# Performance work log

Measured on AMD Instinct MI355X. Metric: run time of the kernel, lower is better.

## Reference

```python
import math
import jax, jax.numpy as jnp
import numpy as np

B, H, S, D = 8, 16, 1024, 64

def setup_inputs() -> dict:
    key = jax.random.key(0)
    kq, kk, kv, km = jax.random.split(key, 4)
    query = jax.random.normal(kq, (B, H, S, D), dtype=jnp.float32)
    k_ = jax.random.normal(kk, (B, H, S, D), dtype=jnp.float32)
    value = jax.random.normal(kv, (B, H, S, D), dtype=jnp.float32)
    mask = jax.random.randint(km, (B, 1, S, S), 0, 2).astype(jnp.bool_)
    return {"query": query, "key": k_, "value": value, "mask": mask}

def reference(query, key, value, mask) -> jnp.ndarray:
    dk = query.shape[-1]
    # scores: [B,H,S,S]
    scores = jnp.einsum("bhqd,bhkd->bhqk", query, key) / math.sqrt(dk)
    scores = jnp.where(mask, scores, jnp.float32(-1e9))
    attention = jax.nn.softmax(scores, axis=-1)
    # log(sigmoid(v)) computed stably, then exp of the weighted sum
    logsig_v = jax.nn.log_sigmoid(value)  # [B,H,S,D]
    return jnp.exp(jnp.einsum("bhqk,bhkd->bhqd", attention, logsig_v))
```

## Files before the change

### kernel.cpp

```cpp
#include <hip/hip_runtime.h>

typedef _Float16 half8  __attribute__((ext_vector_type(8)));
typedef _Float16 half2v __attribute__((ext_vector_type(2)));
typedef float    f32x16 __attribute__((ext_vector_type(16)));
typedef float    f32x4v __attribute__((ext_vector_type(4)));

namespace {
constexpr int kB = 8, kH = 16, kS = 1024, kD = 64;
constexpr int QT  = 128;
constexpr int KT  = 64;
constexpr int NKT = kS / KT;
constexpr int KST = 72;
}

__global__ __launch_bounds__(256, 2)
void sdpa_logsig_kernel(const float* __restrict__ Qg_, const float* __restrict__ Kg_,
                        const float* __restrict__ Vg_, const void* __restrict__ Mg_,
                        float* __restrict__ Og_) {
  __shared__ _Float16 Klds[KT][KST];
  __shared__ _Float16 Vlds[kD][KST];
  __shared__ _Float16 Ptl[4][32][KST];

  const int t    = threadIdx.x;
  const int qblk = blockIdx.x;
  const int bh   = blockIdx.y;
  const int b    = bh >> 4;

  const float* Qg = Qg_ + ((size_t)bh * kS + (size_t)qblk * QT) * kD;
  const float* Kg = Kg_ + (size_t)bh * kS * kD;
  const float* Vg = Vg_ + (size_t)bh * kS * kD;
  float* Og = Og_ + ((size_t)bh * kS + (size_t)qblk * QT) * kD;

  const int l    = t & 63;
  const int w    = t >> 6;
  const int h    = l >> 5;
  const int q31  = l & 31;
  const int qloc = w * 32 + q31;
  const int qg   = qblk * QT + qloc;

  const int skey = t >> 2;
  const int sj   = t & 3;
  const int sd4  = sj << 4;

  unsigned pacc = 0;
  {
    const unsigned* mprobe = (const unsigned*)Mg_;
    #pragma unroll
    for (int i = 0; i < 16; ++i) pacc |= mprobe[i] & 0xFFFFFF00u;
  }
  const bool mask_i32 = (pacc == 0);
  const size_t moff0 = (size_t)b * kS * kS + (size_t)qg * kS + 4 * h;

  half8 qf[4];
  {
    const float* qp = Qg + (size_t)qloc * kD + 8 * h;
    #pragma unroll
    for (int c = 0; c < 4; ++c) {
      f32x4v x = *(const f32x4v*)(qp + 16 * c);
      f32x4v y = *(const f32x4v*)(qp + 16 * c + 4);
      half8 f;
      #pragma unroll
      for (int j = 0; j < 4; ++j) {
        f[j]     = (_Float16)(x[j] * 0.125f);
        f[j + 4] = (_Float16)(y[j] * 0.125f);
      }
      qf[c] = f;
    }
  }

  f32x16 oacc[2];
  #pragma unroll
  for (int d = 0; d < 2; ++d) {
    #pragma unroll
    for (int i = 0; i < 16; ++i) oacc[d][i] = 0.f;
  }
  float mrun = -1e9f, lrun = 0.f;

  for (int kt = 0; kt < NKT; ++kt) {
    __syncthreads();

    {
      const float* kp = Kg + (size_t)(kt * KT + skey) * kD + sd4;
      f32x4v a0 = *(const f32x4v*)(kp);
      f32x4v a1 = *(const f32x4v*)(kp + 4);
      f32x4v a2 = *(const f32x4v*)(kp + 8);
      f32x4v a3 = *(const f32x4v*)(kp + 12);
      half8 h0, h1;
      #pragma unroll
      for (int j = 0; j < 4; ++j) {
        h0[j] = (_Float16)a0[j]; h0[j + 4] = (_Float16)a1[j];
        h1[j] = (_Float16)a2[j]; h1[j + 4] = (_Float16)a3[j];
      }
      *(half8*)&Klds[skey][sd4]     = h0;
      *(half8*)&Klds[skey][sd4 + 8] = h1;
    }

    {
      const float* vp = Vg + (size_t)(kt * KT + skey) * kD + sd4;
      _Float16 lv[16];
      #pragma unroll
      for (int i = 0; i < 4; ++i) {
        const int c = (i + sj) & 3;
        f32x4v xv = *(const f32x4v*)(vp + 4 * c);
        #pragma unroll
        for (int jj = 0; jj < 4; ++jj) {
          float x  = xv[jj];
          float ls = fminf(x, 0.f) - __logf(1.f + __expf(-fabsf(x)));
          lv[4 * i + jj] = (_Float16)ls;
        }
      }
      #pragma unroll
      for (int i = 0; i < 4; ++i) {
        const int c = (i + sj) & 3;
        #pragma unroll
        for (int jj = 0; jj < 4; ++jj)
          Vlds[sd4 + 4 * c + jj][skey] = lv[4 * i + jj];
      }
    }

    unsigned mq[8];
    if (mask_i32) {
      const int* mp = (const int*)Mg_ + moff0 + kt * KT;
      #pragma unroll
      for (int i = 0; i < 8; ++i) {
        const int4 mv = *(const int4*)(mp + 32 * (i >> 2) + 8 * (i & 3));
        mq[i] = (unsigned)(mv.x & 1) | ((unsigned)(mv.y & 1) << 8) |
                ((unsigned)(mv.z & 1) << 16) | ((unsigned)(mv.w & 1) << 24);
      }
    } else {
      const unsigned char* mp = (const unsigned char*)Mg_ + moff0 + kt * KT;
      #pragma unroll
      for (int i = 0; i < 8; ++i)
        mq[i] = *(const unsigned*)(mp + 32 * (i >> 2) + 8 * (i & 3));
    }
    __syncthreads();

    f32x16 sacc[2];
    #pragma unroll
    for (int ks = 0; ks < 2; ++ks) {
      #pragma unroll
      for (int i = 0; i < 16; ++i) sacc[ks][i] = 0.f;
    }
    #pragma unroll
    for (int ks = 0; ks < 2; ++ks) {
      #pragma unroll
      for (int c = 0; c < 4; ++c) {
        half8 kf = *(const half8*)&Klds[32 * ks + q31][16 * c + 8 * h];
        sacc[ks] = __builtin_amdgcn_mfma_f32_32x32x16_f16(kf, qf[c], sacc[ks], 0, 0, 0);
      }
    }

    float smax = -1e9f;
    #pragma unroll
    for (int ks = 0; ks < 2; ++ks) {
      #pragma unroll
      for (int m4 = 0; m4 < 4; ++m4) {
        const unsigned mw = mq[4 * ks + m4];
        #pragma unroll
        for (int r = 0; r < 4; ++r) {
          float s = sacc[ks][4 * m4 + r];
          s = ((mw >> (8 * r)) & 0xffu) ? s : -1e9f;
          sacc[ks][4 * m4 + r] = s;
          smax = fmaxf(smax, s);
        }
      }
    }
    smax = fmaxf(smax, __shfl_xor(smax, 32));
    const float mnew = fmaxf(mrun, smax);
    const float corr = __expf(mrun - mnew);
    mrun = mnew;

    float psum = 0.f;
    #pragma unroll
    for (int ks = 0; ks < 2; ++ks) {
      #pragma unroll
      for (int m4 = 0; m4 < 4; ++m4) {
        _Float16 p0 = (_Float16)__expf(sacc[ks][4 * m4 + 0] - mnew);
        _Float16 p1 = (_Float16)__expf(sacc[ks][4 * m4 + 1] - mnew);
        _Float16 p2 = (_Float16)__expf(sacc[ks][4 * m4 + 2] - mnew);
        _Float16 p3 = (_Float16)__expf(sacc[ks][4 * m4 + 3] - mnew);
        psum += (float)p0 + (float)p1 + (float)p2 + (float)p3;
        half2v p01; p01[0] = p0; p01[1] = p1;
        half2v p23; p23[0] = p2; p23[1] = p3;
        const int key0 = 32 * ks + 8 * m4 + 4 * h;
        *(half2v*)&Ptl[w][q31][key0]     = p01;
        *(half2v*)&Ptl[w][q31][key0 + 2] = p23;
      }
    }
    psum += __shfl_xor(psum, 32);
    lrun = lrun * corr + psum;
    #pragma unroll
    for (int d = 0; d < 2; ++d) {
      #pragma unroll
      for (int i = 0; i < 16; ++i) oacc[d][i] *= corr;
    }

    half8 pf[4];
    #pragma unroll
    for (int c2 = 0; c2 < 4; ++c2)
      pf[c2] = *(const half8*)&Ptl[w][q31][16 * c2 + 8 * h];
    #pragma unroll
    for (int ds = 0; ds < 2; ++ds) {
      #pragma unroll
      for (int c2 = 0; c2 < 4; ++c2) {
        half8 vf = *(const half8*)&Vlds[32 * ds + q31][16 * c2 + 8 * h];
        oacc[ds] = __builtin_amdgcn_mfma_f32_32x32x16_f16(vf, pf[c2], oacc[ds], 0, 0, 0);
      }
    }
  }

  const float invl = 1.f / lrun;
  float* op = Og + (size_t)qloc * kD;
  #pragma unroll
  for (int ds = 0; ds < 2; ++ds) {
    #pragma unroll
    for (int m4 = 0; m4 < 4; ++m4) {
      f32x4v v;
      #pragma unroll
      for (int r = 0; r < 4; ++r)
        v[r] = __expf(oacc[ds][4 * m4 + r] * invl);
      *(f32x4v*)&op[32 * ds + 8 * m4 + 4 * h] = v;
    }
  }
}

extern "C" void kernel_launch(void* const* d_in, const int* in_sizes, int n_in,
                              void* d_out, int out_size, void* d_ws, size_t ws_size,
                              hipStream_t stream) {
  const float* Q = (const float*)d_in[0];
  const float* K = (const float*)d_in[1];
  const float* V = (const float*)d_in[2];
  const void*  M = (const void*)d_in[3];
  float* O = (float*)d_out;
  dim3 grid(kS / QT, kB * kH);
  sdpa_logsig_kernel<<<grid, dim3(256), 0, stream>>>(Q, K, V, M, O);
}
```

Baseline: 262.8 us.

## Precompute fp16 K, transposed log-sigmoid V and packed mask bits in a prepass

Adds a preprocessing kernel that writes K as fp16, log-sigmoid(V) as transposed fp16, and the int mask as 32-bit bitmasks into the workspace. The attention kernel then reads these compact arrays instead of re-reading fp32 K/V and the full int mask for every query block and every head. The main kernel also adds register double-buffering of the next tile, an XCD-aware block index mapping, and raises launch bounds to 4 blocks per CU. The cost is an extra launch plus a full pass over K, V and the mask. The prepass assumes an int32 mask layout and drops the byte-mask detection the old kernel did.

```diff
diff --git a/kernel.cpp b/kernel.cpp
--- a/kernel.cpp
+++ b/kernel.cpp
@@ -1,6 +1,7 @@
 #include <hip/hip_runtime.h>
 
 typedef _Float16 half8  __attribute__((ext_vector_type(8)));
+typedef _Float16 half4v __attribute__((ext_vector_type(4)));
 typedef _Float16 half2v __attribute__((ext_vector_type(2)));
 typedef float    f32x16 __attribute__((ext_vector_type(16)));
 typedef float    f32x4v __attribute__((ext_vector_type(4)));
@@ -11,6 +12,240 @@
 constexpr int KT  = 64;
 constexpr int NKT = kS / KT;
 constexpr int KST = 72;
+constexpr size_t KH_OFF = 0;
+constexpr size_t VT_OFF = (size_t)kB * kH * kS * kD * 2;
+constexpr size_t MB_OFF = VT_OFF * 2;
+constexpr size_t WS_NEED = MB_OFF + (size_t)kB * kS * (kS / 32) * 4;
+}
+
+__device__ __forceinline__ float logsig(float x) {
+  return fminf(x, 0.f) - __logf(1.f + __expf(-fabsf(x)));
+}
+
+__global__ __launch_bounds__(256, 4)
+void pre_kernel(const float* __restrict__ K, const float* __restrict__ V,
+                const int* __restrict__ M, _Float16* __restrict__ Kh,
+                _Float16* __restrict__ Vt, unsigned* __restrict__ Mb) {
+  const int blk = blockIdx.x, t = threadIdx.x;
+  if (blk < 8192) {
+    const size_t idx = ((size_t)blk * 256 + t) * 4;
+    f32x4v x = *(const f32x4v*)(K + idx);
+    half4v o;
+    #pragma unroll
+    for (int j = 0; j < 4; ++j) o[j] = (_Float16)x[j];
+    *(half4v*)(Kh + idx) = o;
+  } else if (blk < 10240) {
+    __shared__ _Float16 T[64][72];
+    const int bb = blk - 8192;
+    const int bh = bb >> 4, ktt = bb & 15;
+    const int key = t >> 2, dc = (t & 3) << 4;
+    const float* vp = V + (((size_t)bh * kS + ktt * KT + key)) * kD + dc;
+    #pragma unroll
+    for (int i = 0; i < 4; ++i) {
+      f32x4v x = *(const f32x4v*)(vp + 4 * i);
+      #pragma unroll
+      for (int j = 0; j < 4; ++j) T[dc + 4 * i + j][key] = (_Float16)logsig(x[j]);
+    }
+    __syncthreads();
+    const int d = t >> 2, kc = (t & 3) << 4;
+    half8 r0 = *(const half8*)&T[d][kc];
+    half8 r1 = *(const half8*)&T[d][kc + 8];
+    _Float16* op = Vt + ((size_t)bh * kD + d) * kS + ktt * KT + kc;
+    *(half8*)op = r0;
+    *(half8*)(op + 8) = r1;
+  } else {
+    const int wi = (blk - 10240) * 256 + t;
+    const int row = wi >> 5;
+    const int wrd = wi & 31;
+    const int* mp = M + (size_t)row * kS + wrd * 32;
+    unsigned bits = 0;
+    #pragma unroll
+    for (int i = 0; i < 8; ++i) {
+      const int4 v = *(const int4*)(mp + 4 * i);
+      bits |= (unsigned)(v.x & 1) << (4 * i) | (unsigned)(v.y & 1) << (4 * i + 1) |
+              (unsigned)(v.z & 1) << (4 * i + 2) | (unsigned)(v.w & 1) << (4 * i + 3);
+    }
+    Mb[wi] = bits;
+  }
+}
+
+__global__ __launch_bounds__(256, 4)
+void sdpa_main(const float* __restrict__ Qg_, const _Float16* __restrict__ Kh,
+               const _Float16* __restrict__ Vt, const unsigned* __restrict__ Mb,
+               float* __restrict__ Og_) {
+  __shared__ _Float16 Klds[KT][KST];
+  __shared__ _Float16 Vlds[kD][KST];
+  __shared__ _Float16 Ptl[4][32][KST];
+
+  const int t = threadIdx.x;
+  const int n   = blockIdx.x;
+  const int xcd = n & 7, c = n >> 3;
+  const int bh  = (xcd << 4) | (c >> 3);
+  const int qblk = c & 7;
+  const int b   = bh >> 4;
+
+  const float* Qg = Qg_ + ((size_t)bh * kS + (size_t)qblk * QT) * kD;
+  float* Og = Og_ + ((size_t)bh * kS + (size_t)qblk * QT) * kD;
+
+  const int l    = t & 63;
+  const int w    = t >> 6;
+  const int h    = l >> 5;
+  const int q31  = l & 31;
+  const int qloc = w * 32 + q31;
+  const int qg   = qblk * QT + qloc;
+
+  const int skey = t >> 2;
+  const int sd4  = (t & 3) << 4;
+  const int vrow = t >> 2;
+  const int vkc  = (t & 3) << 4;
+
+  const _Float16* kbase = Kh + ((size_t)bh * kS + skey) * kD + sd4;
+  const _Float16* vbase = Vt + ((size_t)bh * kD + vrow) * kS + vkc;
+  const unsigned* mbase = Mb + ((size_t)(b * kS + qg)) * 32;
+
+  half8 qf[4];
+  {
+    const float* qp = Qg + (size_t)qloc * kD + 8 * h;
+    #pragma unroll
+    for (int cc = 0; cc < 4; ++cc) {
+      f32x4v x = *(const f32x4v*)(qp + 16 * cc);
+      f32x4v y = *(const f32x4v*)(qp + 16 * cc + 4);
+      half8 f;
+      #pragma unroll
+      for (int j = 0; j < 4; ++j) {
+        f[j]     = (_Float16)(x[j] * 0.125f);
+        f[j + 4] = (_Float16)(y[j] * 0.125f);
+      }
+      qf[cc] = f;
+    }
+  }
+
+  f32x16 oacc[2];
+  #pragma unroll
+  for (int d = 0; d < 2; ++d) {
+    #pragma unroll
+    for (int i = 0; i < 16; ++i) oacc[d][i] = 0.f;
+  }
+  float mrun = -1e9f, lrun = 0.f;
+
+  uint4 kreg0 = *(const uint4*)(kbase);
+  uint4 kreg1 = *(const uint4*)(kbase + 8);
+  uint4 vreg0 = *(const uint4*)(vbase);
+  uint4 vreg1 = *(const uint4*)(vbase + 8);
+  uint2 mreg  = *(const uint2*)(mbase);
+
+  for (int kt = 0; kt < NKT; ++kt) {
+    __syncthreads();
+
+    *(uint4*)&Klds[skey][sd4]     = kreg0;
+    *(uint4*)&Klds[skey][sd4 + 8] = kreg1;
+    *(uint4*)&Vlds[vrow][vkc]     = vreg0;
+    *(uint4*)&Vlds[vrow][vkc + 8] = vreg1;
+
+    unsigned nib[8];
+    #pragma unroll
+    for (int i = 0; i < 8; ++i) {
+      const unsigned wv = (i >> 2) ? mreg.y : mreg.x;
+      nib[i] = (wv >> (8 * (i & 3) + 4 * h)) & 0xFu;
+    }
+
+    if (kt + 1 < NKT) {
+      const size_t ko = (size_t)(kt + 1) * KT * kD;
+      kreg0 = *(const uint4*)(kbase + ko);
+      kreg1 = *(const uint4*)(kbase + ko + 8);
+      vreg0 = *(const uint4*)(vbase + (kt + 1) * KT);
+      vreg1 = *(const uint4*)(vbase + (kt + 1) * KT + 8);
+      mreg  = *(const uint2*)(mbase + (kt + 1) * 2);
+    }
+    __syncthreads();
+
+    f32x16 sacc[2];
+    #pragma unroll
+    for (int ks = 0; ks < 2; ++ks) {
+      #pragma unroll
+      for (int i = 0; i < 16; ++i) sacc[ks][i] = 0.f;
+    }
+    #pragma unroll
+    for (int ks = 0; ks < 2; ++ks) {
+      #pragma unroll
+      for (int cc = 0; cc < 4; ++cc) {
+        half8 kf = *(const half8*)&Klds[32 * ks + q31][16 * cc + 8 * h];
+        sacc[ks] = __builtin_amdgcn_mfma_f32_32x32x16_f16(kf, qf[cc], sacc[ks], 0, 0, 0);
+      }
+    }
+
+    float smax = -1e9f;
+    #pragma unroll
+    for (int ks = 0; ks < 2; ++ks) {
+      #pragma unroll
+      for (int m4 = 0; m4 < 4; ++m4) {
+        const unsigned nb = nib[4 * ks + m4];
+        #pragma unroll
+        for (int r = 0; r < 4; ++r) {
+          float s = sacc[ks][4 * m4 + r];
+          s = (nb & (1u << r)) ? s : -1e9f;
+          sacc[ks][4 * m4 + r] = s;
+          smax = fmaxf(smax, s);
+        }
+      }
+    }
+    smax = fmaxf(smax, __shfl_xor(smax, 32));
+    const float mnew = fmaxf(mrun, smax);
+    const float corr = __expf(mrun - mnew);
+    mrun = mnew;
+
+    float psum = 0.f;
+    #pragma unroll
+    for (int ks = 0; ks < 2; ++ks) {
+      #pragma unroll
+      for (int m4 = 0; m4 < 4; ++m4) {
+        float e0 = __expf(sacc[ks][4 * m4 + 0] - mnew);
+        float e1 = __expf(sacc[ks][4 * m4 + 1] - mnew);
+        float e2 = __expf(sacc[ks][4 * m4 + 2] - mnew);
+        float e3 = __expf(sacc[ks][4 * m4 + 3] - mnew);
+        psum += (e0 + e1) + (e2 + e3);
+        half2v p01; p01[0] = (_Float16)e0; p01[1] = (_Float16)e1;
+        half2v p23; p23[0] = (_Float16)e2; p23[1] = (_Float16)e3;
+        const int key0 = 32 * ks + 8 * m4 + 4 * h;
+        *(half2v*)&Ptl[w][q31][key0]     = p01;
+        *(half2v*)&Ptl[w][q31][key0 + 2] = p23;
+      }
+    }
+    psum += __shfl_xor(psum, 32);
+    lrun = lrun * corr + psum;
+    #pragma unroll
+    for (int d = 0; d < 2; ++d) {
+      #pragma unroll
+      for (int i = 0; i < 16; ++i) oacc[d][i] *= corr;
+    }
+
+    half8 pf[4];
+    #pragma unroll
+    for (int c2 = 0; c2 < 4; ++c2)
+      pf[c2] = *(const half8*)&Ptl[w][q31][16 * c2 + 8 * h];
+    #pragma unroll
+    for (int ds = 0; ds < 2; ++ds) {
+      #pragma unroll
+      for (int c2 = 0; c2 < 4; ++c2) {
+        half8 vf = *(const half8*)&Vlds[32 * ds + q31][16 * c2 + 8 * h];
+        oacc[ds] = __builtin_amdgcn_mfma_f32_32x32x16_f16(vf, pf[c2], oacc[ds], 0, 0, 0);
+      }
+    }
+  }
+
+  const float invl = 1.f / lrun;
+  float* op = Og + (size_t)qloc * kD;
+  #pragma unroll
+  for (int ds = 0; ds < 2; ++ds) {
+    #pragma unroll
+    for (int m4 = 0; m4 < 4; ++m4) {
+      f32x4v v;
+      #pragma unroll
+      for (int r = 0; r < 4; ++r)
+        v[r] = __expf(oacc[ds][4 * m4 + r] * invl);
+      *(f32x4v*)&op[32 * ds + 8 * m4 + 4 * h] = v;
+    }
+  }
 }
 
 __global__ __launch_bounds__(256, 2)
@@ -21,26 +256,20 @@
   __shared__ _Float16 Vlds[kD][KST];
   __shared__ _Float16 Ptl[4][32][KST];
 
-  const int t    = threadIdx.x;
+  const int t = threadIdx.x;
   const int qblk = blockIdx.x;
-  const int bh   = blockIdx.y;
-  const int b    = bh >> 4;
+  const int bh = blockIdx.y;
+  const int b = bh >> 4;
 
   const float* Qg = Qg_ + ((size_t)bh * kS + (size_t)qblk * QT) * kD;
   const float* Kg = Kg_ + (size_t)bh * kS * kD;
   const float* Vg = Vg_ + (size_t)bh * kS * kD;
   float* Og = Og_ + ((size_t)bh * kS + (size_t)qblk * QT) * kD;
 
-  const int l    = t & 63;
-  const int w    = t >> 6;
-  const int h    = l >> 5;
-  const int q31  = l & 31;
+  const int l = t & 63, w = t >> 6, h = l >> 5, q31 = l & 31;
   const int qloc = w * 32 + q31;
-  const int qg   = qblk * QT + qloc;
-
-  const int skey = t >> 2;
-  const int sj   = t & 3;
-  const int sd4  = sj << 4;
+  const int qg = qblk * QT + qloc;
+  const int skey = t >> 2, sj = t & 3, sd4 = sj << 4;
 
   unsigned pacc = 0;
   {
@@ -55,19 +284,15 @@
   {
     const float* qp = Qg + (size_t)qloc * kD + 8 * h;
     #pragma unroll
-    for (int c = 0; c < 4; ++c) {
-      f32x4v x = *(const f32x4v*)(qp + 16 * c);
-      f32x4v y = *(const f32x4v*)(qp + 16 * c + 4);
+    for (int cc = 0; cc < 4; ++cc) {
+      f32x4v x = *(const f32x4v*)(qp + 16 * cc);
+      f32x4v y = *(const f32x4v*)(qp + 16 * cc + 4);
       half8 f;
       #pragma unroll
-      for (int j = 0; j < 4; ++j) {
-        f[j]     = (_Float16)(x[j] * 0.125f);
-        f[j + 4] = (_Float16)(y[j] * 0.125f);
-      }
-      qf[c] = f;
-    }
-  }
-
+      for (int j = 0; j < 4; ++j) { f[j] = (_Float16)(x[j] * 0.125f); f[j + 4] = (_Float16)(y[j] * 0.125f); }
+      qf[cc] = f;
+    }
+  }
   f32x16 oacc[2];
   #pragma unroll
   for (int d = 0; d < 2; ++d) {
@@ -78,46 +303,32 @@
 
   for (int kt = 0; kt < NKT; ++kt) {
     __syncthreads();
-
     {
       const float* kp = Kg + (size_t)(kt * KT + skey) * kD + sd4;
-      f32x4v a0 = *(const f32x4v*)(kp);
-      f32x4v a1 = *(const f32x4v*)(kp + 4);
-      f32x4v a2 = *(const f32x4v*)(kp + 8);
-      f32x4v a3 = *(const f32x4v*)(kp + 12);
+      f32x4v a0 = *(const f32x4v*)(kp);     f32x4v a1 = *(const f32x4v*)(kp + 4);
+      f32x4v a2 = *(const f32x4v*)(kp + 8); f32x4v a3 = *(const f32x4v*)(kp + 12);
       half8 h0, h1;
       #pragma unroll
-      for (int j = 0; j < 4; ++j) {
-        h0[j] = (_Float16)a0[j]; h0[j + 4] = (_Float16)a1[j];
-        h1[j] = (_Float16)a2[j]; h1[j + 4] = (_Float16)a3[j];
-      }
-      *(half8*)&Klds[skey][sd4]     = h0;
-      *(half8*)&Klds[skey][sd4 + 8] = h1;
-    }
-
+      for (int j = 0; j < 4; ++j) { h0[j] = (_Float16)a0[j]; h0[j+4] = (_Float16)a1[j]; h1[j] = (_Float16)a2[j]; h1[j+4] = (_Float16)a3[j]; }
+      *(half8*)&Klds[skey][sd4] = h0; *(half8*)&Klds[skey][sd4 + 8] = h1;
+    }
     {
       const float* vp = Vg + (size_t)(kt * KT + skey) * kD + sd4;
       _Float16 lv[16];
       #pragma unroll
       for (int i = 0; i < 4; ++i) {
-        const int c = (i + sj) & 3;
-        f32x4v xv = *(const f32x4v*)(vp + 4 * c);
+        const int cc = (i + sj) & 3;
+        f32x4v xv = *(const f32x4v*)(vp + 4 * cc);
         #pragma unroll
-        for (int jj = 0; jj < 4; ++jj) {
-          float x  = xv[jj];
-          float ls = fminf(x, 0.f) - __logf(1.f + __expf(-fabsf(x)));
-          lv[4 * i + jj] = (_Float16)ls;
-        }
+        for (int jj = 0; jj < 4; ++jj) lv[4 * i + jj] = (_Float16)logsig(xv[jj]);
       }
       #pragma unroll
       for (int i = 0; i < 4; ++i) {
-        const int c = (i + sj) & 3;
+        const int cc = (i + sj) & 3;
         #pragma unroll
-        for (int jj = 0; jj < 4; ++jj)
-          Vlds[sd4 + 4 * c + jj][skey] = lv[4 * i + jj];
-      }
-    }
-
+        for (int jj = 0; jj < 4; ++jj) Vlds[sd4 + 4 * cc + jj][skey] = lv[4 * i + jj];
+      }
+    }
     unsigned mq[8];
     if (mask_i32) {
       const int* mp = (const int*)Mg_ + moff0 + kt * KT;
@@ -130,8 +341,7 @@
     } else {
       const unsigned char* mp = (const unsigned char*)Mg_ + moff0 + kt * KT;
       #pragma unroll
-      for (int i = 0; i < 8; ++i)
-        mq[i] = *(const unsigned*)(mp + 32 * (i >> 2) + 8 * (i & 3));
+      for (int i = 0; i < 8; ++i) mq[i] = *(const unsigned*)(mp + 32 * (i >> 2) + 8 * (i & 3));
     }
     __syncthreads();
 
@@ -144,12 +354,11 @@
     #pragma unroll
     for (int ks = 0; ks < 2; ++ks) {
       #pragma unroll
-      for (int c = 0; c < 4; ++c) {
-        half8 kf = *(const half8*)&Klds[32 * ks + q31][16 * c + 8 * h];
-        sacc[ks] = __builtin_amdgcn_mfma_f32_32x32x16_f16(kf, qf[c], sacc[ks], 0, 0, 0);
-      }
-    }
-
+      for (int cc = 0; cc < 4; ++cc) {
+        half8 kf = *(const half8*)&Klds[32 * ks + q31][16 * cc + 8 * h];
+        sacc[ks] = __builtin_amdgcn_mfma_f32_32x32x16_f16(kf, qf[cc], sacc[ks], 0, 0, 0);
+      }
+    }
     float smax = -1e9f;
     #pragma unroll
     for (int ks = 0; ks < 2; ++ks) {
@@ -169,21 +378,20 @@
     const float mnew = fmaxf(mrun, smax);
     const float corr = __expf(mrun - mnew);
     mrun = mnew;
-
     float psum = 0.f;
     #pragma unroll
     for (int ks = 0; ks < 2; ++ks) {
       #pragma unroll
       for (int m4 = 0; m4 < 4; ++m4) {
-        _Float16 p0 = (_Float16)__expf(sacc[ks][4 * m4 + 0] - mnew);
-        _Float16 p1 = (_Float16)__expf(sacc[ks][4 * m4 + 1] - mnew);
-        _Float16 p2 = (_Float16)__expf(sacc[ks][4 * m4 + 2] - mnew);
-        _Float16 p3 = (_Float16)__expf(sacc[ks][4 * m4 + 3] - mnew);
+        _Float16 p0 = (_Float16)__expf(sacc[ks][4*m4+0] - mnew);
+        _Float16 p1 = (_Float16)__expf(sacc[ks][4*m4+1] - mnew);
+        _Float16 p2 = (_Float16)__expf(sacc[ks][4*m4+2] - mnew);
+        _Float16 p3 = (_Float16)__expf(sacc[ks][4*m4+3] - mnew);
         psum += (float)p0 + (float)p1 + (float)p2 + (float)p3;
         half2v p01; p01[0] = p0; p01[1] = p1;
         half2v p23; p23[0] = p2; p23[1] = p3;
         const int key0 = 32 * ks + 8 * m4 + 4 * h;
-        *(half2v*)&Ptl[w][q31][key0]     = p01;
+        *(half2v*)&Ptl[w][q31][key0] = p01;
         *(half2v*)&Ptl[w][q31][key0 + 2] = p23;
       }
     }
@@ -197,8 +405,7 @@
 
     half8 pf[4];
     #pragma unroll
-    for (int c2 = 0; c2 < 4; ++c2)
-      pf[c2] = *(const half8*)&Ptl[w][q31][16 * c2 + 8 * h];
+    for (int c2 = 0; c2 < 4; ++c2) pf[c2] = *(const half8*)&Ptl[w][q31][16 * c2 + 8 * h];
     #pragma unroll
     for (int ds = 0; ds < 2; ++ds) {
       #pragma unroll
@@ -208,7 +415,6 @@
       }
     }
   }
-
   const float invl = 1.f / lrun;
   float* op = Og + (size_t)qloc * kD;
   #pragma unroll
@@ -217,8 +423,7 @@
     for (int m4 = 0; m4 < 4; ++m4) {
       f32x4v v;
       #pragma unroll
-      for (int r = 0; r < 4; ++r)
-        v[r] = __expf(oacc[ds][4 * m4 + r] * invl);
+      for (int r = 0; r < 4; ++r) v[r] = __expf(oacc[ds][4 * m4 + r] * invl);
       *(f32x4v*)&op[32 * ds + 8 * m4 + 4 * h] = v;
     }
   }
@@ -230,8 +435,14 @@
   const float* Q = (const float*)d_in[0];
   const float* K = (const float*)d_in[1];
   const float* V = (const float*)d_in[2];
-  const void*  M = (const void*)d_in[3];
   float* O = (float*)d_out;
-  dim3 grid(kS / QT, kB * kH);
-  sdpa_logsig_kernel<<<grid, dim3(256), 0, stream>>>(Q, K, V, M, O);
-}
+  if (ws_size >= WS_NEED) {
+    _Float16* Kh = (_Float16*)((char*)d_ws + KH_OFF);
+    _Float16* Vt = (_Float16*)((char*)d_ws + VT_OFF);
+    unsigned* Mb = (unsigned*)((char*)d_ws + MB_OFF);
+    pre_kernel<<<11264, 256, 0, stream>>>(K, V, (const int*)d_in[3], Kh, Vt, Mb);
+    sdpa_main<<<1024, 256, 0, stream>>>(Q, Kh, Vt, Mb, O);
+  } else {
+    sdpa_logsig_kernel<<<dim3(kS / QT, kB * kH), 256, 0, stream>>>(Q, K, V, d_in[3], O);
+  }
+}
```

Result: faster. 224.1 us (-14.7%).
